# Performance work log

Measured on AMD Instinct MI355X. Metric: run time of the kernel, lower is better.

## Reference

```python
import jax, jax.numpy as jnp
import numpy as np

EPS = 1e-5

def layernorm(x, g, b):
    mu = jnp.mean(x, axis=-1, keepdims=True)
    var = jnp.mean(jnp.square(x - mu), axis=-1, keepdims=True)
    return (x - mu) * jax.lax.rsqrt(var + EPS) * g + b

def setup_inputs() -> dict:
    key = jax.random.key(0)
    ks = jax.random.split(key, 12)
    B, T, C, H = 4, 2048, 1024, 8
    Dh = C // H          # 128
    Dff = 4 * C          # 4096
    s = 0.02
    return {
        "x":     jax.random.normal(ks[0], (B, T, C), jnp.float32),
        "wq":    jax.random.normal(ks[1], (H, C, Dh), jnp.float32) * s,
        "wk":    jax.random.normal(ks[2], (H, C, Dh), jnp.float32) * s,
        "wv":    jax.random.normal(ks[3], (H, C, Dh), jnp.float32) * s,
        "w1":    jax.random.normal(ks[4], (C, Dff), jnp.float32) * s,
        "b1":    jnp.zeros((Dff,), jnp.float32),
        "w2":    jax.random.normal(ks[5], (Dff, C), jnp.float32) * s,
        "b2":    jnp.zeros((C,), jnp.float32),
        "ln1_g": jnp.ones((C,), jnp.float32),
        "ln1_b": jnp.zeros((C,), jnp.float32),
        "ln2_g": jnp.ones((C,), jnp.float32),
        "ln2_b": jnp.zeros((C,), jnp.float32),
    }

def reference(x, wq, wk, wv, w1, b1, w2, b2, ln1_g, ln1_b, ln2_g, ln2_b):
    B, T, C = x.shape
    H, _, Dh = wq.shape
    # --- multi-head self-attention (pre-LN) ---
    h = layernorm(x, ln1_g, ln1_b)
    q = jnp.einsum("btc,hcd->bhtd", h, wq)
    k = jnp.einsum("btc,hcd->bhtd", h, wk)
    v = jnp.einsum("btc,hcd->bhtd", h, wv)
    # NOTE: original multiplies by sqrt(head_size) (not divide) -- kept faithful
    scores = jnp.einsum("bhtd,bhsd->bhts", q, k) * (Dh ** 0.5)
    attn = jax.nn.softmax(scores, axis=-1)
    # dropout(p=0.2) treated as identity (eval mode)
    o = jnp.einsum("bhts,bhsd->bhtd", attn, v)
    # concat heads along last dim: head h fills contiguous slice
    o = o.transpose(0, 2, 1, 3).reshape(B, T, H * Dh)
    x = x + o  # no output projection in original module
    # --- feed-forward (pre-LN) ---
    h2 = layernorm(x, ln2_g, ln2_b)
    ff = jax.nn.relu(h2 @ w1 + b1) @ w2 + b2
    return x + ff
```

## Files before the change

kernel.cpp:

```cpp
#include <hip/hip_runtime.h>
#include <hip/hip_bf16.h>
#include <math.h>

#define B_   4
#define T_   2048
#define C_   1024
#define H_   8
#define DH   128
#define DFF  4096
#define M_   (B_*T_)

typedef __attribute__((ext_vector_type(8))) short bf16x8;
typedef __attribute__((ext_vector_type(4))) float f32x4;
typedef __attribute__((ext_vector_type(2))) unsigned int u32x2;

#define SC2 16.32223094f

__device__ __forceinline__ unsigned short f2bf(float x) {
  union { float f; unsigned u; } v; v.f = x;
  return (unsigned short)((v.u + 0x7fffu + ((v.u >> 16) & 1u)) >> 16);
}
__device__ __forceinline__ float bf2f(unsigned short h) {
  union { unsigned u; float f; } v; v.u = ((unsigned)h) << 16; return v.f;
}

__device__ __forceinline__ f32x4 mfma_bf16(bf16x8 a, bf16x8 b, f32x4 c) {
  return __builtin_amdgcn_mfma_f32_16x16x32_bf16(a, b, c, 0, 0, 0);
}

__device__ __forceinline__ void gll16(const void* g, void* l) {
  __builtin_amdgcn_global_load_lds((const __attribute__((address_space(1))) void*)g,
                                   (__attribute__((address_space(3))) void*)l,
                                   16, 0, 0);
}

__global__ __launch_bounds__(256) void ln_kernel(const float* __restrict__ in,
                                                 const float* __restrict__ g,
                                                 const float* __restrict__ bb,
                                                 unsigned short* __restrict__ h_hi,
                                                 unsigned short* __restrict__ h_lo) {
  __shared__ float red[8];
  const int row = blockIdx.x;
  const int tid = threadIdx.x;
  const float* p = in + (size_t)row * C_;
  const float4 xv = *(const float4*)(p + (tid << 2));
  float s  = xv.x + xv.y + xv.z + xv.w;
  float sq = xv.x*xv.x + xv.y*xv.y + xv.z*xv.z + xv.w*xv.w;
  #pragma unroll
  for (int off = 32; off > 0; off >>= 1) {
    s  += __shfl_xor(s, off);
    sq += __shfl_xor(sq, off);
  }
  if ((tid & 63) == 0) { red[(tid >> 6) * 2] = s; red[(tid >> 6) * 2 + 1] = sq; }
  __syncthreads();
  s  = red[0] + red[2] + red[4] + red[6];
  sq = red[1] + red[3] + red[5] + red[7];
  const float mu  = s * (1.0f / C_);
  const float var = sq * (1.0f / C_) - mu * mu;
  const float rs  = rsqrtf(var + 1e-5f);
  const float4 gv = *(const float4*)(g  + (tid << 2));
  const float4 bv = *(const float4*)(bb + (tid << 2));
  float ov[4];
  ov[0] = (xv.x - mu) * rs * gv.x + bv.x;
  ov[1] = (xv.y - mu) * rs * gv.y + bv.y;
  ov[2] = (xv.z - mu) * rs * gv.z + bv.z;
  ov[3] = (xv.w - mu) * rs * gv.w + bv.w;
  ushort4 hv, lv;
  unsigned short* hp = (unsigned short*)&hv;
  unsigned short* lp = (unsigned short*)&lv;
  #pragma unroll
  for (int j = 0; j < 4; ++j) {
    hp[j] = f2bf(ov[j]);
    lp[j] = f2bf(ov[j] - bf2f(hp[j]));
  }
  *(ushort4*)(h_hi + (size_t)row * C_ + (tid << 2)) = hv;
  *(ushort4*)(h_lo + (size_t)row * C_ + (tid << 2)) = lv;
}

__global__ __launch_bounds__(256) void cvt_t_kernel(const float* __restrict__ in,
                                                    unsigned short* __restrict__ out,
                                                    int R, int CC) {
  __shared__ float tile[32][33];
  const int r0 = blockIdx.y << 5, c0 = blockIdx.x << 5;
  const int tr = threadIdx.x >> 3, tc4 = (threadIdx.x & 7) << 2;
  const float4 vv = *(const float4*)(in + (size_t)(r0 + tr) * CC + c0 + tc4);
  tile[tr][tc4+0] = vv.x; tile[tr][tc4+1] = vv.y;
  tile[tr][tc4+2] = vv.z; tile[tr][tc4+3] = vv.w;
  __syncthreads();
  ushort4 o;
  o.x = f2bf(tile[tc4+0][tr]); o.y = f2bf(tile[tc4+1][tr]);
  o.z = f2bf(tile[tc4+2][tr]); o.w = f2bf(tile[tc4+3][tr]);
  *(ushort4*)(out + (size_t)(c0 + tr) * R + r0 + tc4) = o;
}

__global__ __launch_bounds__(256) void cvt_qkv_kernel(const float* __restrict__ wq,
                                                      const float* __restrict__ wk,
                                                      const float* __restrict__ wv,
                                                      unsigned short* __restrict__ wt_hi,
                                                      unsigned short* __restrict__ wt_lo) {
  const int z = blockIdx.z;
  const int which = z >> 3, head = z & 7;
  const float* in = (which == 0 ? wq : (which == 1 ? wk : wv)) + (size_t)head * C_ * DH;
  unsigned short* oh = wt_hi + (size_t)z * DH * C_;
  unsigned short* ol = wt_lo + (size_t)z * DH * C_;
  __shared__ float tile[32][33];
  const int r0 = blockIdx.y << 5, c0 = blockIdx.x << 5;
  const int tr = threadIdx.x >> 3, tc4 = (threadIdx.x & 7) << 2;
  const float4 vv = *(const float4*)(in + (size_t)(r0 + tr) * DH + c0 + tc4);
  tile[tr][tc4+0] = vv.x; tile[tr][tc4+1] = vv.y;
  tile[tr][tc4+2] = vv.z; tile[tr][tc4+3] = vv.w;
  __syncthreads();
  ushort4 hv, lv;
  unsigned short* hp = (unsigned short*)&hv;
  unsigned short* lp = (unsigned short*)&lv;
  #pragma unroll
  for (int j = 0; j < 4; ++j) {
    const float val = tile[tc4+j][tr];
    hp[j] = f2bf(val);
    lp[j] = f2bf(val - bf2f(hp[j]));
  }
  *(ushort4*)(oh + (size_t)(c0 + tr) * C_ + r0 + tc4) = hv;
  *(ushort4*)(ol + (size_t)(c0 + tr) * C_ + r0 + tc4) = lv;
}


__device__ __forceinline__ void gemm128_split3(
    const unsigned short* __restrict__ Ah, const unsigned short* __restrict__ Al,
    int lda,
    const unsigned short* __restrict__ Bh, const unsigned short* __restrict__ Bl,
    int ldb, int K, f32x4 (&acc)[4][4],
    unsigned short* AhS, unsigned short* AlS,
    unsigned short* BhS, unsigned short* BlS) {
  const int tid  = threadIdx.x;
  const int w    = tid >> 6;
  const int lane = tid & 63;
  const int l15  = lane & 15, quad = lane >> 4;
  const int srow = lane >> 2;
  const int skc  = ((lane & 3) << 3) ^ (((srow >> 1) & 3) << 3);
  const int wm = w & 1, wn = w >> 1;
  const int ro = ((quad ^ ((l15 >> 1) & 3)) << 3);

  for (int k0 = 0; k0 < K; k0 += 32) {
    __syncthreads();
    #pragma unroll
    for (int i = 0; i < 2; ++i) {
      const int seg  = w * 2 + i;
      const int r    = seg * 16 + srow;
      const int lofs = seg * 512 + lane * 8;
      gll16(Ah + (size_t)r * lda + k0 + skc, AhS + lofs);
      gll16(Bh + (size_t)r * ldb + k0 + skc, BhS + lofs);
      gll16(Al + (size_t)r * lda + k0 + skc, AlS + lofs);
      gll16(Bl + (size_t)r * ldb + k0 + skc, BlS + lofs);
    }
    __syncthreads();
    bf16x8 aH[4], bH[4], aL[4], bL[4];
    #pragma unroll
    for (int t = 0; t < 4; ++t) {
      aH[t] = *(const bf16x8*)&AhS[(wm * 64 + t * 16 + l15) * 32 + ro];
      bH[t] = *(const bf16x8*)&BhS[(wn * 64 + t * 16 + l15) * 32 + ro];
      aL[t] = *(const bf16x8*)&AlS[(wm * 64 + t * 16 + l15) * 32 + ro];
      bL[t] = *(const bf16x8*)&BlS[(wn * 64 + t * 16 + l15) * 32 + ro];
    }
    #pragma unroll
    for (int rt = 0; rt < 4; ++rt)
      #pragma unroll
      for (int ct = 0; ct < 4; ++ct) {
        acc[rt][ct] = mfma_bf16(aL[rt], bH[ct], acc[rt][ct]);
        acc[rt][ct] = mfma_bf16(aH[rt], bL[ct], acc[rt][ct]);
        acc[rt][ct] = mfma_bf16(aH[rt], bH[ct], acc[rt][ct]);
      }
  }
}

__device__ __forceinline__ void gemm128_db(
    const unsigned short* __restrict__ Ah, int lda,
    const unsigned short* __restrict__ Bh, int ldb, int K, f32x4 (&acc)[4][4],
    unsigned short (&AS0)[4096], unsigned short (&AS1)[4096],
    unsigned short (&BS0)[4096], unsigned short (&BS1)[4096]) {
  const int tid  = threadIdx.x;
  const int w    = tid >> 6;
  const int lane = tid & 63;
  const int l15  = lane & 15, quad = lane >> 4;
  const int srow = lane >> 2;
  const int skc  = ((lane & 3) << 3) ^ (((srow >> 1) & 3) << 3);
  const int wm = w & 1, wn = w >> 1;
  const int ro = ((quad ^ ((l15 >> 1) & 3)) << 3);
  const int Km = K - 1;

  auto STG = [&](int k0, unsigned short* A, unsigned short* B) {
    #pragma unroll
    for (int i = 0; i < 2; ++i) {
      const int seg  = w * 2 + i;
      const int r    = seg * 16 + srow;
      const int lofs = seg * 512 + lane * 8;
      gll16(Ah + (size_t)r * lda + k0 + skc, A + lofs);
      gll16(Bh + (size_t)r * ldb + k0 + skc, B + lofs);
    }
  };
  auto CMP = [&](const unsigned short* A, const unsigned short* B) {
    bf16x8 aH[4], bH[4];
    #pragma unroll
    for (int t = 0; t < 4; ++t) {
      aH[t] = *(const bf16x8*)&A[(wm * 64 + t * 16 + l15) * 32 + ro];
      bH[t] = *(const bf16x8*)&B[(wn * 64 + t * 16 + l15) * 32 + ro];
    }
    #pragma unroll
    for (int rt = 0; rt < 4; ++rt)
      #pragma unroll
      for (int ct = 0; ct < 4; ++ct)
        acc[rt][ct] = mfma_bf16(aH[rt], bH[ct], acc[rt][ct]);
  };

  STG(0, AS0, BS0);
  for (int k0 = 0; k0 < K; k0 += 64) {
    __syncthreads();
    STG((k0 + 32) & Km, AS1, BS1);
    CMP(AS0, BS0);
    __syncthreads();
    STG((k0 + 64) & Km, AS0, BS0);
    CMP(AS1, BS1);
  }
}

__global__ __launch_bounds__(256) void qkm_kernel(const unsigned short* __restrict__ h_hi,
                                                  const unsigned short* __restrict__ h_lo,
                                                  const unsigned short* __restrict__ wt_hi,
                                                  const unsigned short* __restrict__ wt_lo,
                                                  unsigned short* __restrict__ q_hi,
                                                  unsigned short* __restrict__ q_lo,
                                                  unsigned short* __restrict__ k_hi,
                                                  unsigned short* __restrict__ k_lo) {
  __shared__ __align__(16) unsigned short AhS[4096], AlS[4096];
  __shared__ __align__(16) unsigned short BhS[4096], BlS[4096];
  const int m0 = blockIdx.x << 7;
  const int z  = blockIdx.y;
  const int which = z >> 3, head = z & 7;
  f32x4 acc[4][4];
  #pragma unroll
  for (int i = 0; i < 4; ++i)
    #pragma unroll
    for (int j = 0; j < 4; ++j)
      #pragma unroll
      for (int r = 0; r < 4; ++r) acc[i][j][r] = 0.f;
  gemm128_split3(h_hi + (size_t)m0 * C_, h_lo + (size_t)m0 * C_, C_,
                 wt_hi + (size_t)z * DH * C_, wt_lo + (size_t)z * DH * C_, C_,
                 C_, acc, AhS, AlS, BhS, BlS);
  const int lane = threadIdx.x & 63, w = threadIdx.x >> 6;
  const int l15 = lane & 15, quad = lane >> 4;
  const int wm = w & 1, wn = w >> 1;
  const int bh = (m0 >> 11) * H_ + head;
  const int tbase = (m0 & (T_ - 1)) + wm * 64 + quad * 4;
  if (which == 0) {
    #pragma unroll
    for (int rt = 0; rt < 4; ++rt)
      #pragma unroll
      for (int ct = 0; ct < 4; ++ct) {
        const int d = wn * 64 + ct * 16 + l15;
        #pragma unroll
        for (int r = 0; r < 4; ++r) {
          const int t = tbase + rt * 16 + r;
          const float val = acc[rt][ct][r] * SC2;
          const unsigned short hb = f2bf(val);
          const size_t idx = ((size_t)bh * T_ + t) * DH + d;
          q_hi[idx] = hb;
          q_lo[idx] = f2bf(val - bf2f(hb));
        }
      }
  } else {
    #pragma unroll
    for (int rt = 0; rt < 4; ++rt)
      #pragma unroll
      for (int ct = 0; ct < 4; ++ct) {
        const int d = wn * 64 + ct * 16 + l15;
        #pragma unroll
        for (int r = 0; r < 4; ++r) {
          const int t = tbase + rt * 16 + r;
          const int tt = t & 31;
          const float val = acc[rt][ct][r];
          const unsigned short hb = f2bf(val);
          const size_t idx = (((size_t)bh * 64 + (t >> 5)) * 4 + (d >> 5)) * 1024
                           + (size_t)tt * 32 + ((d & 31) ^ (((tt >> 1) & 3) << 3));
          k_hi[idx] = hb;
          k_lo[idx] = f2bf(val - bf2f(hb));
        }
      }
  }
}

__global__ __launch_bounds__(256) void vm_kernel(const unsigned short* __restrict__ h_hi,
                                                 const unsigned short* __restrict__ wv_hi,
                                                 unsigned short* __restrict__ vimg) {
  __shared__ __align__(16) unsigned short AS0[4096], AS1[4096];
  __shared__ __align__(16) unsigned short BS0[4096], BS1[4096];
  const int m0 = blockIdx.x << 7;
  const int head = blockIdx.y;
  f32x4 acc[4][4];
  #pragma unroll
  for (int i = 0; i < 4; ++i)
    #pragma unroll
    for (int j = 0; j < 4; ++j)
      #pragma unroll
      for (int r = 0; r < 4; ++r) acc[i][j][r] = 0.f;
  gemm128_db(h_hi + (size_t)m0 * C_, C_,
             wv_hi + (size_t)(16 + head) * DH * C_, C_,
             C_, acc, AS0, AS1, BS0, BS1);
  const int lane = threadIdx.x & 63, w = threadIdx.x >> 6;
  const int l15 = lane & 15, quad = lane >> 4;
  const int wm = w & 1, wn = w >> 1;
  const int bh = (m0 >> 11) * H_ + head;
  #pragma unroll
  for (int rt = 0; rt < 4; ++rt)
    #pragma unroll
    for (int ct = 0; ct < 4; ++ct) {
      const int d  = wn * 64 + ct * 16 + l15;
      const int t0 = (m0 & (T_ - 1)) + wm * 64 + rt * 16 + quad * 4;
      const int key = (t0 & 31) ^ (((d >> 1) & 3) << 3);
      ushort4 pk;
      pk.x = f2bf(acc[rt][ct][0]); pk.y = f2bf(acc[rt][ct][1]);
      pk.z = f2bf(acc[rt][ct][2]); pk.w = f2bf(acc[rt][ct][3]);
      *(ushort4*)&vimg[(((size_t)bh * 64 + (t0 >> 5)) * 128 + d) * 32 + key] = pk;
    }
}

__global__ __launch_bounds__(256) void ff1_kernel(const unsigned short* __restrict__ h2,
                                                  const unsigned short* __restrict__ w1t,
                                                  const float* __restrict__ b1,
                                                  unsigned short* __restrict__ ff1) {
  __shared__ __align__(16) unsigned short AS0[4096], AS1[4096];
  __shared__ __align__(16) unsigned short BS0[4096], BS1[4096];
  const int n0 = blockIdx.x << 7;
  const int m0 = blockIdx.y << 7;
  f32x4 acc[4][4];
  #pragma unroll
  for (int i = 0; i < 4; ++i)
    #pragma unroll
    for (int j = 0; j < 4; ++j)
      #pragma unroll
      for (int r = 0; r < 4; ++r) acc[i][j][r] = 0.f;
  gemm128_db(h2 + (size_t)m0 * C_, C_,
             w1t + (size_t)n0 * C_, C_,
             C_, acc, AS0, AS1, BS0, BS1);
  const int lane = threadIdx.x & 63, w = threadIdx.x >> 6;
  const int l15 = lane & 15, quad = lane >> 4;
  const int wm = w & 1, wn = w >> 1;
  #pragma unroll
  for (int rt = 0; rt < 4; ++rt)
    #pragma unroll
    for (int ct = 0; ct < 4; ++ct) {
      const int n = n0 + wn * 64 + ct * 16 + l15;
      const float bias = b1[n];
      #pragma unroll
      for (int r = 0; r < 4; ++r) {
        const int m = m0 + wm * 64 + rt * 16 + quad * 4 + r;
        ff1[(size_t)m * DFF + n] = f2bf(fmaxf(acc[rt][ct][r] + bias, 0.f));
      }
    }
}

__global__ __launch_bounds__(256) void ff2_kernel(const unsigned short* __restrict__ ff1,
                                                  const unsigned short* __restrict__ w2t,
                                                  const float* __restrict__ b2,
                                                  const float* __restrict__ xo,
                                                  float* __restrict__ out) {
  __shared__ __align__(16) unsigned short AS0[4096], AS1[4096];
  __shared__ __align__(16) unsigned short BS0[4096], BS1[4096];
  const int n0 = blockIdx.x << 7;
  const int m0 = blockIdx.y << 7;
  f32x4 acc[4][4];
  #pragma unroll
  for (int i = 0; i < 4; ++i)
    #pragma unroll
    for (int j = 0; j < 4; ++j)
      #pragma unroll
      for (int r = 0; r < 4; ++r) acc[i][j][r] = 0.f;
  gemm128_db(ff1 + (size_t)m0 * DFF, DFF,
             w2t + (size_t)n0 * DFF, DFF,
             DFF, acc, AS0, AS1, BS0, BS1);
  const int lane = threadIdx.x & 63, w = threadIdx.x >> 6;
  const int l15 = lane & 15, quad = lane >> 4;
  const int wm = w & 1, wn = w >> 1;
  #pragma unroll
  for (int rt = 0; rt < 4; ++rt)
    #pragma unroll
    for (int ct = 0; ct < 4; ++ct) {
      const int n = n0 + wn * 64 + ct * 16 + l15;
      const float bias = b2[n];
      #pragma unroll
      for (int r = 0; r < 4; ++r) {
        const int m = m0 + wm * 64 + rt * 16 + quad * 4 + r;
        out[(size_t)m * C_ + n] = acc[rt][ct][r] + bias + xo[(size_t)m * C_ + n];
      }
    }
}

#define BQ 128

__global__ __launch_bounds__(256, 2) void attn_kernel(
    const unsigned short* __restrict__ q_hi, const unsigned short* __restrict__ q_lo,
    const unsigned short* __restrict__ k_hi, const unsigned short* __restrict__ k_lo,
    const unsigned short* __restrict__ vimg,
    const float* __restrict__ x, float* __restrict__ xo) {
  __shared__ __align__(16) unsigned short Kh0[4096], Kh1[4096];
  __shared__ __align__(16) unsigned short Kl0[4096], Kl1[4096];
  __shared__ __align__(16) unsigned short Vt0[4096], Vt1[4096];
  __shared__ __align__(16) unsigned short PS [4096];

  const int bid   = blockIdx.x + (T_ / BQ) * blockIdx.y;
  const int chunk = bid >> 3;
  const int bh    = (bid & 7) * 4 + (chunk >> 4);
  const int qt0   = (chunk & 15) * BQ;

  const int tid  = threadIdx.x;
  const int w    = tid >> 6;
  const int lane = tid & 63;
  const int l15  = lane & 15;
  const int quad = lane >> 4;
  const int swz  = (l15 >> 1) & 3;
  const int srcbase = quad * 20;

  bf16x8 Qh[2][4], Ql[2][4];
  #pragma unroll
  for (int rt = 0; rt < 2; ++rt) {
    const int row = qt0 + w * 32 + rt * 16 + l15;
    #pragma unroll
    for (int kc = 0; kc < 4; ++kc) {
      const size_t off = ((size_t)bh * T_ + row) * DH + kc * 32 + quad * 8;
      Qh[rt][kc] = *(const bf16x8*)(q_hi + off);
      Ql[rt][kc] = *(const bf16x8*)(q_lo + off);
    }
  }

  f32x4 O[2][8];
  #pragma unroll
  for (int rt = 0; rt < 2; ++rt)
    #pragma unroll
    for (int n = 0; n < 8; ++n)
      #pragma unroll
      for (int r = 0; r < 4; ++r) O[rt][n][r] = 0.f;
  float m_cur[2] = { -1e30f, -1e30f };
  float l_cur[2] = { 0.f, 0.f };

  auto STAGE = [&](int kt, unsigned short* KH, unsigned short* KL,
                   unsigned short* VT) {
    const size_t tb = ((size_t)bh * 64 + kt) * 4096;
    #pragma unroll
    for (int i = 0; i < 2; ++i) {
      const int ofs = (w * 2 + i) * 512 + lane * 8;
      gll16(k_hi + tb + ofs, KH + ofs);
      gll16(k_lo + tb + ofs, KL + ofs);
      gll16(vimg + tb + ofs, VT + ofs);
    }
  };

  auto TILE = [&](const unsigned short* KH, const unsigned short* KL,
                  const unsigned short* VT) {
    f32x4 S[2][2];
    #pragma unroll
    for (int ct = 0; ct < 2; ++ct)
      #pragma unroll
      for (int rt = 0; rt < 2; ++rt)
        #pragma unroll
        for (int r = 0; r < 4; ++r) S[ct][rt][r] = 0.f;
    __builtin_amdgcn_s_setprio(1);
    #pragma unroll
    for (int kc = 0; kc < 4; ++kc) {
      #pragma unroll
      for (int ct = 0; ct < 2; ++ct) {
        const int o = kc * 1024 + (ct * 16 + l15) * 32 + ((quad ^ swz) << 3);
        const bf16x8 kh = *(const bf16x8*)&KH[o];
        const bf16x8 kl = *(const bf16x8*)&KL[o];
        #pragma unroll
        for (int rt = 0; rt < 2; ++rt) {
          S[ct][rt] = mfma_bf16(kl, Qh[rt][kc], S[ct][rt]);
          S[ct][rt] = mfma_bf16(kh, Ql[rt][kc], S[ct][rt]);
          S[ct][rt] = mfma_bf16(kh, Qh[rt][kc], S[ct][rt]);
        }
      }
    }
    __builtin_amdgcn_s_setprio(0);

    float mx[2];
    #pragma unroll
    for (int rt = 0; rt < 2; ++rt) {
      const float a = fmaxf(fmaxf(S[0][rt][0], S[0][rt][1]),
                            fmaxf(S[0][rt][2], S[0][rt][3]));
      const float b = fmaxf(fmaxf(S[1][rt][0], S[1][rt][1]),
                            fmaxf(S[1][rt][2], S[1][rt][3]));
      float m0 = fmaxf(a, b);
      m0 = fmaxf(m0, __shfl_xor(m0, 16));
      m0 = fmaxf(m0, __shfl_xor(m0, 32));
      mx[rt] = m0;
    }

    const int need = (mx[0] > m_cur[0] + 8.f) || (mx[1] > m_cur[1] + 8.f);
    if (__any(need)) {
      #pragma unroll
      for (int rt = 0; rt < 2; ++rt) {
        const float mn = fmaxf(m_cur[rt], mx[rt]);
        const float al = exp2f(m_cur[rt] - mn);
        m_cur[rt] = mn;
        l_cur[rt] *= al;
        #pragma unroll
        for (int r = 0; r < 4; ++r) {
          const float ar = __shfl(al, srcbase + r);
          #pragma unroll
          for (int n = 0; n < 8; ++n) O[rt][n][r] *= ar;
        }
      }
    }

    #pragma unroll
    for (int rt = 0; rt < 2; ++rt) {
      const int rowb = (w * 32 + rt * 16 + l15) * 64;
      float rs = 0.f;
      #pragma unroll
      for (int ct = 0; ct < 2; ++ct) {
        const float p0 = exp2f(S[ct][rt][0] - m_cur[rt]);
        const float p1 = exp2f(S[ct][rt][1] - m_cur[rt]);
        const float p2 = exp2f(S[ct][rt][2] - m_cur[rt]);
        const float p3 = exp2f(S[ct][rt][3] - m_cur[rt]);
        rs += (p0 + p1) + (p2 + p3);
        u32x2 uu;
        uu.x = (__float_as_uint(p1) & 0xffff0000u) | (__float_as_uint(p0) >> 16);
        uu.y = (__float_as_uint(p3) & 0xffff0000u) | (__float_as_uint(p2) >> 16);
        const int slot = (ct * 2 + (quad >> 1)) ^ swz;
        *(u32x2*)((char*)PS + rowb + (slot << 4) + ((quad & 1) << 3)) = uu;
      }
      rs += __shfl_xor(rs, 16);
      rs += __shfl_xor(rs, 32);
      l_cur[rt] += rs;
    }

    bf16x8 aP[2];
    #pragma unroll
    for (int rt = 0; rt < 2; ++rt) {
      const int rowb = (w * 32 + rt * 16 + l15) * 64;
      aP[rt] = *(const bf16x8*)((const char*)PS + rowb + ((quad ^ swz) << 4));
    }
    __builtin_amdgcn_s_setprio(1);
    #pragma unroll
    for (int n = 0; n < 8; ++n) {
      const int o = (n * 16 + l15) * 32 + ((quad ^ swz) << 3);
      const bf16x8 bv = *(const bf16x8*)&VT[o];
      O[0][n] = mfma_bf16(aP[0], bv, O[0][n]);
      O[1][n] = mfma_bf16(aP[1], bv, O[1][n]);
    }
    __builtin_amdgcn_s_setprio(0);
  };

  STAGE(0, Kh0, Kl0, Vt0);
  for (int j = 0; j < T_ / 64; ++j) {
    const int kt = j * 2;
    __syncthreads();
    STAGE(kt + 1, Kh1, Kl1, Vt1);
    TILE(Kh0, Kl0, Vt0);
    __syncthreads();
    STAGE((kt + 2) & 63, Kh0, Kl0, Vt0);
    TILE(Kh1, Kl1, Vt1);
  }

  const int b = bh >> 3, hh = bh & 7;
  #pragma unroll
  for (int rt = 0; rt < 2; ++rt) {
    #pragma unroll
    for (int r = 0; r < 4; ++r) {
      const float lr = __shfl(l_cur[rt], srcbase + r);
      const float inv_l = 1.0f / lr;
      const int t = qt0 + w * 32 + rt * 16 + quad * 4 + r;
      const size_t xrow = ((size_t)(b * T_ + t)) * C_ + (size_t)hh * DH;
      #pragma unroll
      for (int n = 0; n < 8; ++n) {
        const int d = n * 16 + l15;
        xo[xrow + d] = x[xrow + d] + O[rt][n][r] * inv_l;
      }
    }
  }
}

extern "C" void kernel_launch(void* const* d_in, const int* in_sizes, int n_in,
                              void* d_out, int out_size, void* d_ws, size_t ws_size,
                              hipStream_t stream) {
  (void)in_sizes; (void)n_in; (void)out_size; (void)ws_size;
  const float* x     = (const float*)d_in[0];
  const float* wq    = (const float*)d_in[1];
  const float* wk    = (const float*)d_in[2];
  const float* wv    = (const float*)d_in[3];
  const float* w1    = (const float*)d_in[4];
  const float* b1    = (const float*)d_in[5];
  const float* w2    = (const float*)d_in[6];
  const float* b2    = (const float*)d_in[7];
  const float* ln1_g = (const float*)d_in[8];
  const float* ln1_b = (const float*)d_in[9];
  const float* ln2_g = (const float*)d_in[10];
  const float* ln2_b = (const float*)d_in[11];
  float* out = (float*)d_out;

  char* W = (char*)d_ws;
  float* xo = (float*)(W);
  unsigned short* q_hi  = (unsigned short*)(W + (32u  << 20));
  unsigned short* q_lo  = (unsigned short*)(W + (48u  << 20));
  unsigned short* k_hi  = (unsigned short*)(W + (64u  << 20));
  unsigned short* k_lo  = (unsigned short*)(W + (80u  << 20));
  unsigned short* vimg  = (unsigned short*)(W + (96u  << 20));
  unsigned short* ff1   = (unsigned short*)(W + (32u  << 20));
  unsigned short* h_hi  = (unsigned short*)(W + (112u << 20));
  unsigned short* h_lo  = (unsigned short*)(W + (128u << 20));
  unsigned short* w1t   = (unsigned short*)(W + (144u << 20));
  unsigned short* w2t   = (unsigned short*)(W + (152u << 20));
  unsigned short* wt_hi = (unsigned short*)(W + (160u << 20));
  unsigned short* wt_lo = (unsigned short*)(W + (166u << 20));

  cvt_t_kernel<<<dim3(DFF / 32, C_ / 32), 256, 0, stream>>>(w1, w1t, C_, DFF);
  cvt_t_kernel<<<dim3(C_ / 32, DFF / 32), 256, 0, stream>>>(w2, w2t, DFF, C_);
  cvt_qkv_kernel<<<dim3(DH / 32, C_ / 32, 24), 256, 0, stream>>>(wq, wk, wv, wt_hi, wt_lo);
  ln_kernel<<<M_, 256, 0, stream>>>(x, ln1_g, ln1_b, h_hi, h_lo);
  qkm_kernel<<<dim3(M_ / 128, 16), 256, 0, stream>>>(h_hi, h_lo, wt_hi, wt_lo,
                                                     q_hi, q_lo, k_hi, k_lo);
  vm_kernel<<<dim3(M_ / 128, H_), 256, 0, stream>>>(h_hi, wt_hi, vimg);
  attn_kernel<<<dim3(T_ / BQ, B_ * H_), 256, 0, stream>>>(q_hi, q_lo, k_hi, k_lo,
                                                          vimg, x, xo);
  ln_kernel<<<M_, 256, 0, stream>>>(xo, ln2_g, ln2_b, h_hi, h_lo);
  ff1_kernel<<<dim3(DFF / 128, M_ / 128), 256, 0, stream>>>(h_hi, w1t, b1, ff1);
  ff2_kernel<<<dim3(C_ / 128, M_ / 128), 256, 0, stream>>>(ff1, w2t, b2, xo, out);
}
```

Before: 632.1 us.

## Restructure attention to 8 waves with 16 query rows and register P shuffle

Attention blocks now use 512 threads, each wave owning 16 query rows instead of 32, and each iteration processes a 64-key tile (two 32-key K halves) before one softmax update. The P matrix is redistributed across lanes with shuffles instead of a round trip through shared memory, so the PS buffer is gone, and V is staged as 64-key double buffers. The aim is more waves per CU for latency hiding, fewer softmax/rescale passes, and less LDS traffic. The cost is more barriers per iteration, a larger V buffer, and more cross-lane shuffle instructions.

Result: faster. 618.5 us (-2.2%).

```diff
diff --git a/kernel.cpp b/kernel.cpp
--- a/kernel.cpp
+++ b/kernel.cpp
@@ -395,15 +395,14 @@
 
 #define BQ 128
 
-__global__ __launch_bounds__(256, 2) void attn_kernel(
+__global__ __launch_bounds__(512, 4) void attn_kernel(
     const unsigned short* __restrict__ q_hi, const unsigned short* __restrict__ q_lo,
     const unsigned short* __restrict__ k_hi, const unsigned short* __restrict__ k_lo,
     const unsigned short* __restrict__ vimg,
     const float* __restrict__ x, float* __restrict__ xo) {
   __shared__ __align__(16) unsigned short Kh0[4096], Kh1[4096];
   __shared__ __align__(16) unsigned short Kl0[4096], Kl1[4096];
-  __shared__ __align__(16) unsigned short Vt0[4096], Vt1[4096];
-  __shared__ __align__(16) unsigned short PS [4096];
+  __shared__ __align__(16) unsigned short Vt0[8192], Vt1[8192];
 
   const int bid   = blockIdx.x + (T_ / BQ) * blockIdx.y;
   const int chunk = bid >> 3;
@@ -417,162 +416,159 @@
   const int quad = lane >> 4;
   const int swz  = (l15 >> 1) & 3;
   const int srcbase = quad * 20;
-
-  bf16x8 Qh[2][4], Ql[2][4];
-  #pragma unroll
-  for (int rt = 0; rt < 2; ++rt) {
-    const int row = qt0 + w * 32 + rt * 16 + l15;
+  const int sA   = ((quad & 1) << 5) + l15;
+  const int sB   = sA + 16;
+  const int bsel = (quad >> 1) & 1;
+
+  bf16x8 Qh[4], Ql[4];
+  {
+    const int row = qt0 + w * 16 + l15;
     #pragma unroll
     for (int kc = 0; kc < 4; ++kc) {
       const size_t off = ((size_t)bh * T_ + row) * DH + kc * 32 + quad * 8;
-      Qh[rt][kc] = *(const bf16x8*)(q_hi + off);
-      Ql[rt][kc] = *(const bf16x8*)(q_lo + off);
-    }
-  }
-
-  f32x4 O[2][8];
-  #pragma unroll
-  for (int rt = 0; rt < 2; ++rt)
-    #pragma unroll
-    for (int n = 0; n < 8; ++n)
-      #pragma unroll
-      for (int r = 0; r < 4; ++r) O[rt][n][r] = 0.f;
-  float m_cur[2] = { -1e30f, -1e30f };
-  float l_cur[2] = { 0.f, 0.f };
-
-  auto STAGE = [&](int kt, unsigned short* KH, unsigned short* KL,
-                   unsigned short* VT) {
+      Qh[kc] = *(const bf16x8*)(q_hi + off);
+      Ql[kc] = *(const bf16x8*)(q_lo + off);
+    }
+  }
+
+  f32x4 O[8];
+  #pragma unroll
+  for (int n = 0; n < 8; ++n)
+    #pragma unroll
+    for (int r = 0; r < 4; ++r) O[n][r] = 0.f;
+  float m_cur = -1e30f;
+  float l_cur = 0.f;
+
+  auto STAGE_K = [&](int kt, unsigned short* KH, unsigned short* KL) {
     const size_t tb = ((size_t)bh * 64 + kt) * 4096;
+    const int ofs = w * 512 + lane * 8;
+    gll16(k_hi + tb + ofs, KH + ofs);
+    gll16(k_lo + tb + ofs, KL + ofs);
+  };
+  auto STAGE_V = [&](int jv, unsigned short* VT) {
+    const size_t tb = ((size_t)bh * 64 + jv * 2) * 4096;
     #pragma unroll
     for (int i = 0; i < 2; ++i) {
-      const int ofs = (w * 2 + i) * 512 + lane * 8;
-      gll16(k_hi + tb + ofs, KH + ofs);
-      gll16(k_lo + tb + ofs, KL + ofs);
-      gll16(vimg + tb + ofs, VT + ofs);
+      const int o = (w * 2 + i) * 512 + lane * 8;
+      gll16(vimg + tb + o, VT + o);
     }
   };
-
-  auto TILE = [&](const unsigned short* KH, const unsigned short* KL,
-                  const unsigned short* VT) {
-    f32x4 S[2][2];
-    #pragma unroll
-    for (int ct = 0; ct < 2; ++ct)
-      #pragma unroll
-      for (int rt = 0; rt < 2; ++rt)
-        #pragma unroll
-        for (int r = 0; r < 4; ++r) S[ct][rt][r] = 0.f;
+  auto QKT = [&](const unsigned short* KH, const unsigned short* KL, f32x4* Sp) {
     __builtin_amdgcn_s_setprio(1);
     #pragma unroll
-    for (int kc = 0; kc < 4; ++kc) {
+    for (int kc = 0; kc < 4; ++kc)
       #pragma unroll
       for (int ct = 0; ct < 2; ++ct) {
         const int o = kc * 1024 + (ct * 16 + l15) * 32 + ((quad ^ swz) << 3);
         const bf16x8 kh = *(const bf16x8*)&KH[o];
         const bf16x8 kl = *(const bf16x8*)&KL[o];
-        #pragma unroll
-        for (int rt = 0; rt < 2; ++rt) {
-          S[ct][rt] = mfma_bf16(kl, Qh[rt][kc], S[ct][rt]);
-          S[ct][rt] = mfma_bf16(kh, Ql[rt][kc], S[ct][rt]);
-          S[ct][rt] = mfma_bf16(kh, Qh[rt][kc], S[ct][rt]);
-        }
-      }
-    }
-    __builtin_amdgcn_s_setprio(0);
-
-    float mx[2];
-    #pragma unroll
-    for (int rt = 0; rt < 2; ++rt) {
-      const float a = fmaxf(fmaxf(S[0][rt][0], S[0][rt][1]),
-                            fmaxf(S[0][rt][2], S[0][rt][3]));
-      const float b = fmaxf(fmaxf(S[1][rt][0], S[1][rt][1]),
-                            fmaxf(S[1][rt][2], S[1][rt][3]));
-      float m0 = fmaxf(a, b);
-      m0 = fmaxf(m0, __shfl_xor(m0, 16));
-      m0 = fmaxf(m0, __shfl_xor(m0, 32));
-      mx[rt] = m0;
-    }
-
-    const int need = (mx[0] > m_cur[0] + 8.f) || (mx[1] > m_cur[1] + 8.f);
-    if (__any(need)) {
-      #pragma unroll
-      for (int rt = 0; rt < 2; ++rt) {
-        const float mn = fmaxf(m_cur[rt], mx[rt]);
-        const float al = exp2f(m_cur[rt] - mn);
-        m_cur[rt] = mn;
-        l_cur[rt] *= al;
-        #pragma unroll
-        for (int r = 0; r < 4; ++r) {
-          const float ar = __shfl(al, srcbase + r);
-          #pragma unroll
-          for (int n = 0; n < 8; ++n) O[rt][n][r] *= ar;
-        }
-      }
-    }
-
-    #pragma unroll
-    for (int rt = 0; rt < 2; ++rt) {
-      const int rowb = (w * 32 + rt * 16 + l15) * 64;
-      float rs = 0.f;
-      #pragma unroll
-      for (int ct = 0; ct < 2; ++ct) {
-        const float p0 = exp2f(S[ct][rt][0] - m_cur[rt]);
-        const float p1 = exp2f(S[ct][rt][1] - m_cur[rt]);
-        const float p2 = exp2f(S[ct][rt][2] - m_cur[rt]);
-        const float p3 = exp2f(S[ct][rt][3] - m_cur[rt]);
-        rs += (p0 + p1) + (p2 + p3);
-        u32x2 uu;
-        uu.x = (__float_as_uint(p1) & 0xffff0000u) | (__float_as_uint(p0) >> 16);
-        uu.y = (__float_as_uint(p3) & 0xffff0000u) | (__float_as_uint(p2) >> 16);
-        const int slot = (ct * 2 + (quad >> 1)) ^ swz;
-        *(u32x2*)((char*)PS + rowb + (slot << 4) + ((quad & 1) << 3)) = uu;
-      }
-      rs += __shfl_xor(rs, 16);
-      rs += __shfl_xor(rs, 32);
-      l_cur[rt] += rs;
-    }
-
-    bf16x8 aP[2];
-    #pragma unroll
-    for (int rt = 0; rt < 2; ++rt) {
-      const int rowb = (w * 32 + rt * 16 + l15) * 64;
-      aP[rt] = *(const bf16x8*)((const char*)PS + rowb + ((quad ^ swz) << 4));
-    }
-    __builtin_amdgcn_s_setprio(1);
-    #pragma unroll
-    for (int n = 0; n < 8; ++n) {
-      const int o = (n * 16 + l15) * 32 + ((quad ^ swz) << 3);
-      const bf16x8 bv = *(const bf16x8*)&VT[o];
-      O[0][n] = mfma_bf16(aP[0], bv, O[0][n]);
-      O[1][n] = mfma_bf16(aP[1], bv, O[1][n]);
-    }
+        Sp[ct] = mfma_bf16(kl, Qh[kc], Sp[ct]);
+        Sp[ct] = mfma_bf16(kh, Ql[kc], Sp[ct]);
+        Sp[ct] = mfma_bf16(kh, Qh[kc], Sp[ct]);
+      }
     __builtin_amdgcn_s_setprio(0);
   };
 
-  STAGE(0, Kh0, Kl0, Vt0);
+  STAGE_K(0, Kh0, Kl0);
+  STAGE_K(1, Kh1, Kl1);
+  STAGE_V(0, Vt0);
+
   for (int j = 0; j < T_ / 64; ++j) {
-    const int kt = j * 2;
+    const unsigned short* Vc = (j & 1) ? Vt1 : Vt0;
+    unsigned short*       Vn = (j & 1) ? Vt0 : Vt1;
+
     __syncthreads();
-    STAGE(kt + 1, Kh1, Kl1, Vt1);
-    TILE(Kh0, Kl0, Vt0);
+    f32x4 S[4];
+    #pragma unroll
+    for (int ct = 0; ct < 4; ++ct)
+      #pragma unroll
+      for (int r = 0; r < 4; ++r) S[ct][r] = 0.f;
+    QKT(Kh0, Kl0, &S[0]);
     __syncthreads();
-    STAGE((kt + 2) & 63, Kh0, Kl0, Vt0);
-    TILE(Kh1, Kl1, Vt1);
+    STAGE_K((2 * j + 2) & 63, Kh0, Kl0);
+    STAGE_V((j + 1) & 31, Vn);
+    QKT(Kh1, Kl1, &S[2]);
+    __syncthreads();
+    STAGE_K((2 * j + 3) & 63, Kh1, Kl1);
+
+    float mx = -1e30f;
+    #pragma unroll
+    for (int ct = 0; ct < 4; ++ct)
+      mx = fmaxf(mx, fmaxf(fmaxf(S[ct][0], S[ct][1]), fmaxf(S[ct][2], S[ct][3])));
+    mx = fmaxf(mx, __shfl_xor(mx, 16));
+    mx = fmaxf(mx, __shfl_xor(mx, 32));
+
+    if (__any(mx > m_cur + 8.f)) {
+      const float mn = fmaxf(m_cur, mx);
+      const float al = exp2f(m_cur - mn);
+      m_cur = mn;
+      l_cur *= al;
+      #pragma unroll
+      for (int r = 0; r < 4; ++r) {
+        const float ar = __shfl(al, srcbase + r);
+        #pragma unroll
+        for (int n = 0; n < 8; ++n) O[n][r] *= ar;
+      }
+    }
+
+    unsigned pu[8];
+    float rs = 0.f;
+    #pragma unroll
+    for (int ct = 0; ct < 4; ++ct) {
+      const float p0 = exp2f(S[ct][0] - m_cur);
+      const float p1 = exp2f(S[ct][1] - m_cur);
+      const float p2 = exp2f(S[ct][2] - m_cur);
+      const float p3 = exp2f(S[ct][3] - m_cur);
+      rs += (p0 + p1) + (p2 + p3);
+      pu[ct * 2 + 0] = (__float_as_uint(p1) & 0xffff0000u) | (__float_as_uint(p0) >> 16);
+      pu[ct * 2 + 1] = (__float_as_uint(p3) & 0xffff0000u) | (__float_as_uint(p2) >> 16);
+    }
+    rs += __shfl_xor(rs, 16);
+    rs += __shfl_xor(rs, 32);
+    l_cur += rs;
+
+    bf16x8 aP[2];
+    #pragma unroll
+    for (int g = 0; g < 2; ++g) {
+      const unsigned xA0 = (unsigned)__shfl((int)pu[4 * g + 0], sA);
+      const unsigned yA0 = (unsigned)__shfl((int)pu[4 * g + 2], sA);
+      const unsigned xA1 = (unsigned)__shfl((int)pu[4 * g + 1], sA);
+      const unsigned yA1 = (unsigned)__shfl((int)pu[4 * g + 3], sA);
+      const unsigned xB0 = (unsigned)__shfl((int)pu[4 * g + 0], sB);
+      const unsigned yB0 = (unsigned)__shfl((int)pu[4 * g + 2], sB);
+      const unsigned xB1 = (unsigned)__shfl((int)pu[4 * g + 1], sB);
+      const unsigned yB1 = (unsigned)__shfl((int)pu[4 * g + 3], sB);
+      union { unsigned u[4]; bf16x8 v; } cv;
+      cv.u[0] = bsel ? yA0 : xA0;
+      cv.u[1] = bsel ? yA1 : xA1;
+      cv.u[2] = bsel ? yB0 : xB0;
+      cv.u[3] = bsel ? yB1 : xB1;
+      aP[g] = cv.v;
+    }
+
+    __builtin_amdgcn_s_setprio(1);
+    #pragma unroll
+    for (int g = 0; g < 2; ++g)
+      #pragma unroll
+      for (int n = 0; n < 8; ++n) {
+        const bf16x8 bv =
+            *(const bf16x8*)&Vc[g * 4096 + (n * 16 + l15) * 32 + ((quad ^ swz) << 3)];
+        O[n] = mfma_bf16(aP[g], bv, O[n]);
+      }
+    __builtin_amdgcn_s_setprio(0);
   }
 
   const int b = bh >> 3, hh = bh & 7;
   #pragma unroll
-  for (int rt = 0; rt < 2; ++rt) {
-    #pragma unroll
-    for (int r = 0; r < 4; ++r) {
-      const float lr = __shfl(l_cur[rt], srcbase + r);
-      const float inv_l = 1.0f / lr;
-      const int t = qt0 + w * 32 + rt * 16 + quad * 4 + r;
-      const size_t xrow = ((size_t)(b * T_ + t)) * C_ + (size_t)hh * DH;
-      #pragma unroll
-      for (int n = 0; n < 8; ++n) {
-        const int d = n * 16 + l15;
-        xo[xrow + d] = x[xrow + d] + O[rt][n][r] * inv_l;
-      }
+  for (int r = 0; r < 4; ++r) {
+    const float lr = __shfl(l_cur, srcbase + r);
+    const float inv_l = 1.0f / lr;
+    const int t = qt0 + w * 16 + quad * 4 + r;
+    const size_t xrow = ((size_t)(b * T_ + t)) * C_ + (size_t)hh * DH;
+    #pragma unroll
+    for (int n = 0; n < 8; ++n) {
+      const int d = n * 16 + l15;
+      xo[xrow + d] = x[xrow + d] + O[n][r] * inv_l;
     }
   }
 }
@@ -617,7 +613,7 @@
   qkm_kernel<<<dim3(M_ / 128, 16), 256, 0, stream>>>(h_hi, h_lo, wt_hi, wt_lo,
                                                      q_hi, q_lo, k_hi, k_lo);
   vm_kernel<<<dim3(M_ / 128, H_), 256, 0, stream>>>(h_hi, wt_hi, vimg);
-  attn_kernel<<<dim3(T_ / BQ, B_ * H_), 256, 0, stream>>>(q_hi, q_lo, k_hi, k_lo,
+  attn_kernel<<<dim3(T_ / BQ, B_ * H_), 512, 0, stream>>>(q_hi, q_lo, k_hi, k_lo,
                                                           vimg, x, xo);
   ln_kernel<<<M_, 256, 0, stream>>>(xo, ln2_g, ln2_b, h_hi, h_lo);
   ff1_kernel<<<dim3(DFF / 128, M_ / 128), 256, 0, stream>>>(h_hi, w1t, b1, ff1);
```

## Enlarge attention query tile to 256 rows and pass P via register shuffles

Applied to the files above, without the earlier changes.

The attention kernel now uses 512 threads and a 256-row query tile, so each staged K/V tile is shared by more queries. It processes 64 keys per softmax step with separately double-buffered K and V stages. The P matrix now moves from the score layout into the PV MFMA operand through lane shuffles instead of a shared-memory round trip, and the PV MFMA operands are swapped so the output layout allows float4 stores to xo. The aims are less global/LDS traffic per query and fewer LDS writes and reads; the costs are more shuffle instructions, a larger block per CU, and half as many blocks (256).

New measurement: 612.8 us. 3.1% less time.

```diff
diff --git a/kernel.cpp b/kernel.cpp
--- a/kernel.cpp
+++ b/kernel.cpp
@@ -393,22 +393,21 @@
     }
 }
 
-#define BQ 128
-
-__global__ __launch_bounds__(256, 2) void attn_kernel(
+#define BQ 256
+
+__global__ __launch_bounds__(512, 2) void attn_kernel(
     const unsigned short* __restrict__ q_hi, const unsigned short* __restrict__ q_lo,
     const unsigned short* __restrict__ k_hi, const unsigned short* __restrict__ k_lo,
     const unsigned short* __restrict__ vimg,
     const float* __restrict__ x, float* __restrict__ xo) {
   __shared__ __align__(16) unsigned short Kh0[4096], Kh1[4096];
   __shared__ __align__(16) unsigned short Kl0[4096], Kl1[4096];
-  __shared__ __align__(16) unsigned short Vt0[4096], Vt1[4096];
-  __shared__ __align__(16) unsigned short PS [4096];
+  __shared__ __align__(16) unsigned short Vt0[8192], Vt1[8192];
 
   const int bid   = blockIdx.x + (T_ / BQ) * blockIdx.y;
   const int chunk = bid >> 3;
-  const int bh    = (bid & 7) * 4 + (chunk >> 4);
-  const int qt0   = (chunk & 15) * BQ;
+  const int bh    = (bid & 7) * 4 + (chunk >> 3);
+  const int qt0   = (chunk & 7) * BQ;
 
   const int tid  = threadIdx.x;
   const int w    = tid >> 6;
@@ -416,7 +415,9 @@
   const int l15  = lane & 15;
   const int quad = lane >> 4;
   const int swz  = (l15 >> 1) & 3;
-  const int srcbase = quad * 20;
+  const int sA   = ((quad & 1) << 5) + l15;
+  const int sB   = sA + 16;
+  const int bsel = (quad >> 1) & 1;
 
   bf16x8 Qh[2][4], Ql[2][4];
   #pragma unroll
@@ -440,58 +441,72 @@
   float m_cur[2] = { -1e30f, -1e30f };
   float l_cur[2] = { 0.f, 0.f };
 
-  auto STAGE = [&](int kt, unsigned short* KH, unsigned short* KL,
-                   unsigned short* VT) {
-    const size_t tb = ((size_t)bh * 64 + kt) * 4096;
-    #pragma unroll
-    for (int i = 0; i < 2; ++i) {
-      const int ofs = (w * 2 + i) * 512 + lane * 8;
-      gll16(k_hi + tb + ofs, KH + ofs);
-      gll16(k_lo + tb + ofs, KL + ofs);
-      gll16(vimg + tb + ofs, VT + ofs);
-    }
+  auto STAGE_K = [&](int kt, unsigned short* KH, unsigned short* KL) {
+    const size_t tb = ((size_t)bh * 64 + (kt & 63)) * 4096;
+    const int o = tid * 8;
+    gll16(k_hi + tb + o, KH + o);
+    gll16(k_lo + tb + o, KL + o);
   };
-
-  auto TILE = [&](const unsigned short* KH, const unsigned short* KL,
-                  const unsigned short* VT) {
-    f32x4 S[2][2];
-    #pragma unroll
-    for (int ct = 0; ct < 2; ++ct)
-      #pragma unroll
-      for (int rt = 0; rt < 2; ++rt)
-        #pragma unroll
-        for (int r = 0; r < 4; ++r) S[ct][rt][r] = 0.f;
+  auto STAGE_V = [&](int jv, unsigned short* VT) {
+    const size_t tb = ((size_t)bh * 64 + (jv & 31) * 2) * 4096;
+    const int o = tid * 8;
+    gll16(vimg + tb + o, VT + o);
+    gll16(vimg + tb + 4096 + o, VT + 4096 + o);
+  };
+  auto QKT = [&](const unsigned short* KH, const unsigned short* KL,
+                 f32x4 (&S2)[2][2]) {
     __builtin_amdgcn_s_setprio(1);
     #pragma unroll
-    for (int kc = 0; kc < 4; ++kc) {
-      #pragma unroll
-      for (int ct = 0; ct < 2; ++ct) {
-        const int o = kc * 1024 + (ct * 16 + l15) * 32 + ((quad ^ swz) << 3);
+    for (int kc = 0; kc < 4; ++kc)
+      #pragma unroll
+      for (int c2 = 0; c2 < 2; ++c2) {
+        const int o = kc * 1024 + (c2 * 16 + l15) * 32 + ((quad ^ swz) << 3);
         const bf16x8 kh = *(const bf16x8*)&KH[o];
         const bf16x8 kl = *(const bf16x8*)&KL[o];
         #pragma unroll
         for (int rt = 0; rt < 2; ++rt) {
-          S[ct][rt] = mfma_bf16(kl, Qh[rt][kc], S[ct][rt]);
-          S[ct][rt] = mfma_bf16(kh, Ql[rt][kc], S[ct][rt]);
-          S[ct][rt] = mfma_bf16(kh, Qh[rt][kc], S[ct][rt]);
+          S2[c2][rt] = mfma_bf16(kl, Qh[rt][kc], S2[c2][rt]);
+          S2[c2][rt] = mfma_bf16(kh, Ql[rt][kc], S2[c2][rt]);
+          S2[c2][rt] = mfma_bf16(kh, Qh[rt][kc], S2[c2][rt]);
         }
       }
-    }
     __builtin_amdgcn_s_setprio(0);
+  };
+
+  STAGE_K(0, Kh0, Kl0);
+  STAGE_K(1, Kh1, Kl1);
+  STAGE_V(0, Vt0);
+
+  for (int j = 0; j < T_ / 64; ++j) {
+    __syncthreads();
+    f32x4 S[4][2];
+    #pragma unroll
+    for (int ct = 0; ct < 4; ++ct)
+      #pragma unroll
+      for (int rt = 0; rt < 2; ++rt)
+        #pragma unroll
+        for (int r = 0; r < 4; ++r) S[ct][rt][r] = 0.f;
+
+    QKT(Kh0, Kl0, *(f32x4 (*)[2][2])&S[0]);
+    __syncthreads();
+    STAGE_K(2 * j + 2, Kh0, Kl0);
+    STAGE_V(j + 1, (j & 1) ? Vt0 : Vt1);
+    QKT(Kh1, Kl1, *(f32x4 (*)[2][2])&S[2]);
+    __syncthreads();
+    STAGE_K(2 * j + 3, Kh1, Kl1);
 
     float mx[2];
     #pragma unroll
     for (int rt = 0; rt < 2; ++rt) {
-      const float a = fmaxf(fmaxf(S[0][rt][0], S[0][rt][1]),
-                            fmaxf(S[0][rt][2], S[0][rt][3]));
-      const float b = fmaxf(fmaxf(S[1][rt][0], S[1][rt][1]),
-                            fmaxf(S[1][rt][2], S[1][rt][3]));
-      float m0 = fmaxf(a, b);
+      float m0 = -1e30f;
+      #pragma unroll
+      for (int ct = 0; ct < 4; ++ct)
+        m0 = fmaxf(m0, fmaxf(fmaxf(S[ct][rt][0], S[ct][rt][1]),
+                             fmaxf(S[ct][rt][2], S[ct][rt][3])));
       m0 = fmaxf(m0, __shfl_xor(m0, 16));
       m0 = fmaxf(m0, __shfl_xor(m0, 32));
       mx[rt] = m0;
     }
-
     const int need = (mx[0] > m_cur[0] + 8.f) || (mx[1] > m_cur[1] + 8.f);
     if (__any(need)) {
       #pragma unroll
@@ -501,78 +516,81 @@
         m_cur[rt] = mn;
         l_cur[rt] *= al;
         #pragma unroll
-        for (int r = 0; r < 4; ++r) {
-          const float ar = __shfl(al, srcbase + r);
+        for (int n = 0; n < 8; ++n)
           #pragma unroll
-          for (int n = 0; n < 8; ++n) O[rt][n][r] *= ar;
-        }
-      }
-    }
-
+          for (int r = 0; r < 4; ++r) O[rt][n][r] *= al;
+      }
+    }
+
+    bf16x8 bP[2][2];
     #pragma unroll
     for (int rt = 0; rt < 2; ++rt) {
-      const int rowb = (w * 32 + rt * 16 + l15) * 64;
+      unsigned pu[8];
       float rs = 0.f;
       #pragma unroll
-      for (int ct = 0; ct < 2; ++ct) {
+      for (int ct = 0; ct < 4; ++ct) {
         const float p0 = exp2f(S[ct][rt][0] - m_cur[rt]);
         const float p1 = exp2f(S[ct][rt][1] - m_cur[rt]);
         const float p2 = exp2f(S[ct][rt][2] - m_cur[rt]);
         const float p3 = exp2f(S[ct][rt][3] - m_cur[rt]);
         rs += (p0 + p1) + (p2 + p3);
-        u32x2 uu;
-        uu.x = (__float_as_uint(p1) & 0xffff0000u) | (__float_as_uint(p0) >> 16);
-        uu.y = (__float_as_uint(p3) & 0xffff0000u) | (__float_as_uint(p2) >> 16);
-        const int slot = (ct * 2 + (quad >> 1)) ^ swz;
-        *(u32x2*)((char*)PS + rowb + (slot << 4) + ((quad & 1) << 3)) = uu;
+        pu[ct * 2 + 0] = (__float_as_uint(p1) & 0xffff0000u) | (__float_as_uint(p0) >> 16);
+        pu[ct * 2 + 1] = (__float_as_uint(p3) & 0xffff0000u) | (__float_as_uint(p2) >> 16);
       }
       rs += __shfl_xor(rs, 16);
       rs += __shfl_xor(rs, 32);
       l_cur[rt] += rs;
-    }
-
-    bf16x8 aP[2];
-    #pragma unroll
-    for (int rt = 0; rt < 2; ++rt) {
-      const int rowb = (w * 32 + rt * 16 + l15) * 64;
-      aP[rt] = *(const bf16x8*)((const char*)PS + rowb + ((quad ^ swz) << 4));
-    }
-    __builtin_amdgcn_s_setprio(1);
+      #pragma unroll
+      for (int g = 0; g < 2; ++g) {
+        const unsigned xA0 = (unsigned)__shfl((int)pu[4 * g + 0], sA);
+        const unsigned yA0 = (unsigned)__shfl((int)pu[4 * g + 2], sA);
+        const unsigned xA1 = (unsigned)__shfl((int)pu[4 * g + 1], sA);
+        const unsigned yA1 = (unsigned)__shfl((int)pu[4 * g + 3], sA);
+        const unsigned xB0 = (unsigned)__shfl((int)pu[4 * g + 0], sB);
+        const unsigned yB0 = (unsigned)__shfl((int)pu[4 * g + 2], sB);
+        const unsigned xB1 = (unsigned)__shfl((int)pu[4 * g + 1], sB);
+        const unsigned yB1 = (unsigned)__shfl((int)pu[4 * g + 3], sB);
+        union { unsigned u[4]; bf16x8 v; } cv;
+        cv.u[0] = bsel ? yA0 : xA0;
+        cv.u[1] = bsel ? yA1 : xA1;
+        cv.u[2] = bsel ? yB0 : xB0;
+        cv.u[3] = bsel ? yB1 : xB1;
+        bP[rt][g] = cv.v;
+      }
+    }
+
+    {
+      const unsigned short* VT = (j & 1) ? Vt1 : Vt0;
+      __builtin_amdgcn_s_setprio(1);
+      #pragma unroll
+      for (int g = 0; g < 2; ++g)
+        #pragma unroll
+        for (int n = 0; n < 8; ++n) {
+          const bf16x8 av =
+              *(const bf16x8*)&VT[g * 4096 + (n * 16 + l15) * 32 + ((quad ^ swz) << 3)];
+          O[0][n] = mfma_bf16(av, bP[0][g], O[0][n]);
+          O[1][n] = mfma_bf16(av, bP[1][g], O[1][n]);
+        }
+      __builtin_amdgcn_s_setprio(0);
+    }
+  }
+
+  const int b = bh >> 3, hh = bh & 7;
+  #pragma unroll
+  for (int rt = 0; rt < 2; ++rt) {
+    const float inv_l = 1.0f / l_cur[rt];
+    const int t = qt0 + w * 32 + rt * 16 + l15;
+    const size_t xrow = ((size_t)(b * T_ + t)) * C_ + (size_t)hh * DH;
     #pragma unroll
     for (int n = 0; n < 8; ++n) {
-      const int o = (n * 16 + l15) * 32 + ((quad ^ swz) << 3);
-      const bf16x8 bv = *(const bf16x8*)&VT[o];
-      O[0][n] = mfma_bf16(aP[0], bv, O[0][n]);
-      O[1][n] = mfma_bf16(aP[1], bv, O[1][n]);
-    }
-    __builtin_amdgcn_s_setprio(0);
-  };
-
-  STAGE(0, Kh0, Kl0, Vt0);
-  for (int j = 0; j < T_ / 64; ++j) {
-    const int kt = j * 2;
-    __syncthreads();
-    STAGE(kt + 1, Kh1, Kl1, Vt1);
-    TILE(Kh0, Kl0, Vt0);
-    __syncthreads();
-    STAGE((kt + 2) & 63, Kh0, Kl0, Vt0);
-    TILE(Kh1, Kl1, Vt1);
-  }
-
-  const int b = bh >> 3, hh = bh & 7;
-  #pragma unroll
-  for (int rt = 0; rt < 2; ++rt) {
-    #pragma unroll
-    for (int r = 0; r < 4; ++r) {
-      const float lr = __shfl(l_cur[rt], srcbase + r);
-      const float inv_l = 1.0f / lr;
-      const int t = qt0 + w * 32 + rt * 16 + quad * 4 + r;
-      const size_t xrow = ((size_t)(b * T_ + t)) * C_ + (size_t)hh * DH;
-      #pragma unroll
-      for (int n = 0; n < 8; ++n) {
-        const int d = n * 16 + l15;
-        xo[xrow + d] = x[xrow + d] + O[rt][n][r] * inv_l;
-      }
+      const int d = n * 16 + quad * 4;
+      const float4 xv = *(const float4*)(x + xrow + d);
+      float4 ov;
+      ov.x = xv.x + O[rt][n][0] * inv_l;
+      ov.y = xv.y + O[rt][n][1] * inv_l;
+      ov.z = xv.z + O[rt][n][2] * inv_l;
+      ov.w = xv.w + O[rt][n][3] * inv_l;
+      *(float4*)(xo + xrow + d) = ov;
     }
   }
 }
@@ -617,7 +635,7 @@
   qkm_kernel<<<dim3(M_ / 128, 16), 256, 0, stream>>>(h_hi, h_lo, wt_hi, wt_lo,
                                                      q_hi, q_lo, k_hi, k_lo);
   vm_kernel<<<dim3(M_ / 128, H_), 256, 0, stream>>>(h_hi, wt_hi, vimg);
-  attn_kernel<<<dim3(T_ / BQ, B_ * H_), 256, 0, stream>>>(q_hi, q_lo, k_hi, k_lo,
+  attn_kernel<<<dim3(T_ / BQ, B_ * H_), 512, 0, stream>>>(q_hi, q_lo, k_hi, k_lo,
                                                           vimg, x, xo);
   ln_kernel<<<M_, 256, 0, stream>>>(xo, ln2_g, ln2_b, h_hi, h_lo);
   ff1_kernel<<<dim3(DFF / 128, M_ / 128), 256, 0, stream>>>(h_hi, w1t, b1, ff1);
```
